# Optimization experiments

Measured on AMD Instinct MI355X. Metric: run time of the kernel, lower is better.

The kernel has to match this reference:

```python
import jax, jax.numpy as jnp
import numpy as np

STEPS = 4
EMB = 128
HEADS = 3
NUM_GRAPHS = 64
NODES_PER = 64
N = NUM_GRAPHS * NODES_PER
E_SPARSE = N * 16
DATA_LENS = [NODES_PER] * NUM_GRAPHS


def _complete_edge_index(data_lens):
    # dense_to_sparse(complete_matrix) -> all (i,j) pairs within each block,
    # including self loops (diagonal of complete_matrix is 1).
    srcs, dsts = [], []
    start = 0
    for l in data_lens:
        idx = np.arange(start, start + l)
        srcs.append(np.repeat(idx, l))
        dsts.append(np.tile(idx, l))
        start += l
    return np.stack([np.concatenate(srcs), np.concatenate(dsts)]).astype(np.int32)


def leaky(x, slope=0.01):
    return jnp.where(x >= 0, x, slope * x)


def setup_inputs() -> dict:
    key = jax.random.key(0)
    ks = jax.random.split(key, 16)
    s = 0.05
    edge_complete = jnp.asarray(_complete_edge_index(DATA_LENS))
    # sparse edge_index: random edges within each graph
    src_local = jax.random.randint(ks[1], (E_SPARSE,), 0, NODES_PER)
    dst_local = jax.random.randint(ks[2], (E_SPARSE,), 0, NODES_PER)
    gid = jnp.repeat(jnp.arange(NUM_GRAPHS), E_SPARSE // NUM_GRAPHS) * NODES_PER
    edge_index = jnp.stack([src_local + gid, dst_local + gid]).astype(jnp.int32)
    batch_ind = jnp.repeat(jnp.arange(NUM_GRAPHS), NODES_PER).astype(jnp.int32)
    return {
        "x": jax.random.normal(ks[0], (N, EMB), jnp.float32),
        "edge_index": edge_index,
        "batch_ind": batch_ind,
        "edge_complete": edge_complete,
        "Wm": jax.random.normal(ks[3], (STEPS, EMB, EMB)) * s,
        "bm": jnp.zeros((STEPS, EMB)),
        "Wa": jax.random.normal(ks[4], (STEPS, 3 * EMB, EMB)) * s,
        "ba": jnp.zeros((STEPS, EMB)),
        "Wl": jax.random.normal(ks[5], (STEPS - 1, EMB, HEADS * EMB)) * s,
        "bl": jnp.zeros((STEPS - 1, HEADS * EMB)),
        "Wr": jax.random.normal(ks[6], (STEPS - 1, EMB, HEADS * EMB)) * s,
        "br": jnp.zeros((STEPS - 1, HEADS * EMB)),
        "att_w": jax.random.normal(ks[7], (STEPS - 1, HEADS, EMB)) * s,
        "att_bias": jnp.zeros((STEPS - 1, EMB)),
    }


def _graphnet(x, x_att, batch_ind, src, dst, Wm, bm, Wa, ba):
    # message: f_mess(x_j)  (edge_attr is None in this model)
    m = leaky(x[src] @ Wm + bm)                               # [E, D]
    agg = jax.ops.segment_max(m, dst, num_segments=x.shape[0])
    agg = jnp.where(jnp.isneginf(agg), 0.0, agg)              # PyG fills empty with 0
    xg = x_att[batch_ind]                                     # [N, D]
    z = jnp.concatenate([x, xg, agg], axis=1)                 # [N, 3D]
    return leaky(z @ Wa + ba) + x


def _gatv2(x, src, dst, Wl, bl, Wr, br, att, bias):
    n = x.shape[0]
    xl = (x @ Wl + bl).reshape(n, HEADS, EMB)                 # source transform
    xr = (x @ Wr + br).reshape(n, HEADS, EMB)                 # target transform
    e = leaky(xl[src] + xr[dst], 0.2)                         # [E, H, D]
    logits = jnp.einsum('ehd,hd->eh', e, att)                 # [E, H]
    mx = jax.ops.segment_max(logits, dst, num_segments=n)
    mx = jnp.where(jnp.isneginf(mx), 0.0, mx)
    alpha = jnp.exp(logits - mx[dst])
    denom = jax.ops.segment_sum(alpha, dst, num_segments=n)
    alpha = alpha / denom[dst]                                # softmax over incoming edges
    out = jax.ops.segment_sum(alpha[:, :, None] * xl[src], dst, num_segments=n)
    return out.mean(axis=1) + bias                            # concat=False -> head mean


def reference(x, edge_index, batch_ind, edge_complete, Wm, bm, Wa, ba, Wl, bl, Wr, br, att_w, att_bias):
    src, dst = edge_index[0], edge_index[1]
    csrc, cdst = edge_complete[0], edge_complete[1]
    x_att = jnp.zeros((NUM_GRAPHS, EMB), x.dtype)
    for i in range(STEPS):
        x = _graphnet(x, x_att, batch_ind, src, dst, Wm[i], bm[i], Wa[i], ba[i])
        if i < STEPS - 1:
            x_att_nodes = leaky(_gatv2(x, csrc, cdst, Wl[i], bl[i], Wr[i], br[i], att_w[i], att_bias[i]))
            # original indexes xg = x_att[batch_ind]; x_att here is per-node, so
            # emulate torch semantics: x_att has len(x) rows, indexed by batch_ind.
            x_att = x_att_nodes
        # note: in original, x_att has shape [len(x), emb]; xg = x_att[batch_ind]
    return x


if __name__ == "__main__":
    out = reference(**setup_inputs())
    print(out.shape)
```

## Files before the change

### kernel.cpp

```cpp
#include <hip/hip_runtime.h>
#include <math.h>

#define D 128
#define GB 64
#define BT 1024
#define ZP 264
#define XLP 74

typedef __attribute__((ext_vector_type(8))) short bf16x8;
typedef __attribute__((ext_vector_type(4))) float f32x4;
typedef __attribute__((ext_vector_type(4))) unsigned u32x4;

__device__ __forceinline__ float leaky01(float v) { return v >= 0.f ? v : 0.01f * v; }
__device__ __forceinline__ unsigned short f2bf(float f) {
    unsigned u = __float_as_uint(f);
    u += 0x7FFFu + ((u >> 16) & 1u);
    return (unsigned short)(u >> 16);
}
__device__ __forceinline__ float bf2f(unsigned short s) {
    return __uint_as_float(((unsigned)s) << 16);
}

__device__ __forceinline__ void st_sys_u32(unsigned* p, unsigned v) {
    asm volatile("global_store_dword %0, %1, off sc0 sc1" :: "v"(p), "v"(v) : "memory");
}
__device__ __forceinline__ void st_sys_u128(unsigned* p, u32x4 v) {
    asm volatile("global_store_dwordx4 %0, %1, off sc0 sc1" :: "v"(p), "v"(v) : "memory");
}
__device__ __forceinline__ unsigned ld_sys_u32(const unsigned* p) {
    unsigned v;
    asm volatile("global_load_dword %0, %1, off sc0 sc1\n\ts_waitcnt vmcnt(0)"
                 : "=v"(v) : "v"(p) : "memory");
    return v;
}
__device__ __forceinline__ u32x4 ld_sys_u128(const unsigned* p) {
    u32x4 v;
    asm volatile("global_load_dwordx4 %0, %1, off sc0 sc1\n\ts_waitcnt vmcnt(0)"
                 : "=v"(v) : "v"(p) : "memory");
    return v;
}
__device__ __forceinline__ void waitst() { asm volatile("s_waitcnt vmcnt(0)" ::: "memory"); }

__global__ void k_wconv(const float* __restrict__ Wm, const float* __restrict__ Wa,
                        const float* __restrict__ Wl, const float* __restrict__ Wr,
                        unsigned short* __restrict__ Wmt, unsigned short* __restrict__ Wat,
                        unsigned short* __restrict__ Wlt, unsigned short* __restrict__ Wrt,
                        unsigned* __restrict__ flags) {
    int gid = blockIdx.x * blockDim.x + threadIdx.x;
    if (blockIdx.x == 0 && threadIdx.x < 8) st_sys_u32(&flags[threadIdx.x], 0u);
    if (gid < 16384) {
        int o = gid * 4;
        int s = o >> 14, rem = o & 16383, n = rem >> 7, k0 = rem & 127;
        const float* src = Wm + (size_t)s * 16384;
        unsigned short* dst = Wmt + o;
#pragma unroll
        for (int j = 0; j < 4; ++j) dst[j] = f2bf(src[(size_t)(k0 + j) * 128 + n]);
    } else if (gid < 49152) {
        int o = (gid - 16384) * 4;
        int s = o >> 15, rem = o & 32767, n = rem >> 8, k0 = rem & 255;
        int row = (k0 < 128) ? k0 : (k0 + 128);
        const float* src = Wa + (size_t)s * 49152;
        unsigned short* dst = Wat + o;
#pragma unroll
        for (int j = 0; j < 4; ++j) dst[j] = f2bf(src[(size_t)(row + j) * 128 + n]);
    } else if (gid < 86016) {
        int o = (gid - 49152) * 4;
        int s = o / 49152, rem = o % 49152, n = rem >> 7, k0 = rem & 127;
        const float* src = Wl + (size_t)s * 49152;
        unsigned short* dst = Wlt + o;
#pragma unroll
        for (int j = 0; j < 4; ++j) dst[j] = f2bf(src[(size_t)(k0 + j) * 384 + n]);
    } else if (gid < 122880) {
        int o = (gid - 86016) * 4;
        unsigned short* dst = Wrt + o;
#pragma unroll
        for (int j = 0; j < 4; ++j) dst[j] = f2bf(Wr[(size_t)o + j]);
    }
}

struct Args {
    const float* x0;
    const int* e_src; const int* e_dst;
    const unsigned short *Wmt, *Wat, *Wlt, *Wrt;
    const float *Wa, *bm, *ba, *bl, *br, *att_w, *att_bias;
    unsigned short* xg0;
    unsigned* flagX;
    float* out;
};

__global__ __launch_bounds__(BT) void k_mega(Args p) {
    const int tid = threadIdx.x, bid = blockIdx.x, g = bid;
    const int wave = tid >> 6, lane = tid & 63;
    const int m16 = lane & 15, kg = lane >> 4;
    const int wtile = wave >> 1;
    const int half = wave & 1;
    const int col = wtile * 16 + m16;

    __shared__ unsigned short zsb[64][ZP];
    __shared__ unsigned short hs[64][128];
    __shared__ unsigned short xl3[3][128][XLP];
    __shared__ float red[4608];
    __shared__ unsigned mlo[64], mhi[64];
    __shared__ float att_s[3][D];
    __shared__ float br_s[384];
    __shared__ float xgrow[D];

    unsigned short (*xg_s)[128] = (unsigned short(*)[128])&hs[0][0];

    if (tid < 64) { mlo[tid] = 0u; mhi[tid] = 0u; }
    __syncthreads();
    {
        int i0 = g * 1024 + tid;
        int s1 = p.e_src[i0] - g * 64, d1 = p.e_dst[i0] - g * 64;
        atomicOr(s1 < 32 ? &mlo[d1] : &mhi[d1], 1u << (s1 & 31));
    }

    float xreg[8];
    {
        const float* xp = p.x0 + (size_t)g * 64 * D;
#pragma unroll
        for (int i = 0; i < 2; ++i) {
            int mt = half * 2 + i;
#pragma unroll
            for (int r = 0; r < 4; ++r)
                xreg[i * 4 + r] = xp[(mt * 16 + kg * 4 + r) * D + col];
        }
    }
    __syncthreads();

    for (int step = 0; step < 4; ++step) {
        if (step > 0 && tid < 128) {
            float accO = red[3840 + tid] + red[3840 + 128 + tid] + red[3840 + 256 + tid]
                       + red[3840 + 384 + tid] + red[3840 + 512 + tid] + red[3840 + 640 + tid];
            xgrow[tid] = leaky01(accO * (1.f / 3.f) + p.att_bias[(step - 1) * 128 + tid]);
        }
#pragma unroll
        for (int i = 0; i < 2; ++i) {
            int mt = half * 2 + i;
#pragma unroll
            for (int r = 0; r < 4; ++r) zsb[mt * 16 + kg * 4 + r][col] = f2bf(xreg[i * 4 + r]);
        }
        if (step < 3 && tid < 384) {
            att_s[tid >> 7][tid & 127] = p.att_w[step * 384 + tid];
            br_s[tid] = p.br[step * 384 + tid];
        }
        __syncthreads();

        {
            const unsigned short* Wb = p.Wmt + ((size_t)(step * 128 + col) * 128 + kg * 8);
            bf16x8 bB[4];
#pragma unroll
            for (int kt = 0; kt < 4; ++kt) bB[kt] = *(const bf16x8*)(Wb + kt * 32);
            float bb = p.bm[step * 128 + col];
#pragma unroll
            for (int i = 0; i < 2; ++i) {
                int mt = half * 2 + i;
                f32x4 acc = {0.f, 0.f, 0.f, 0.f};
#pragma unroll
                for (int kt = 0; kt < 4; ++kt) {
                    bf16x8 a = *(const bf16x8*)&zsb[mt * 16 + m16][kt * 32 + kg * 8];
                    acc = __builtin_amdgcn_mfma_f32_16x16x32_bf16(a, bB[kt], acc, 0, 0, 0);
                }
#pragma unroll
                for (int r = 0; r < 4; ++r)
                    hs[mt * 16 + kg * 4 + r][col] = f2bf(leaky01(acc[r] + bb));
            }
        }
        __syncthreads();

        bf16x8 wat[8];
        {
            const unsigned short* WbU = p.Wat + ((size_t)(step * 128 + col) * 256 + kg * 8);
#pragma unroll
            for (int kt = 0; kt < 8; ++kt) wat[kt] = *(const bf16x8*)(WbU + kt * 32);
        }
        if (step > 0) {
            int n = tid & 127, q = tid >> 7;
            float a = 0.f;
            const float* Wmid = p.Wa + (size_t)step * 49152 + (size_t)(128 + q * 16) * 128 + n;
#pragma unroll 8
            for (int k2 = 0; k2 < 16; ++k2) a += xgrow[q * 16 + k2] * Wmid[(size_t)k2 * 128];
            red[q * 128 + n] = a;
        }
        {
            int r0 = wave * 4;
#pragma unroll
            for (int r = 0; r < 4; ++r) {
                int row = r0 + r;
                unsigned lo = (unsigned)__builtin_amdgcn_readfirstlane((int)mlo[row]);
                unsigned hi = (unsigned)__builtin_amdgcn_readfirstlane((int)mhi[row]);
                unsigned long long mk = (((unsigned long long)hi) << 32) | lo;
                float m0 = -INFINITY, m1 = -INFINITY;
                unsigned long long t = mk;
                while (t) {
                    int s = __builtin_ctzll(t);
                    t &= t - 1;
                    unsigned hv = *(const unsigned*)&hs[s][lane * 2];
                    m0 = fmaxf(m0, bf2f((unsigned short)(hv & 0xffffu)));
                    m1 = fmaxf(m1, bf2f((unsigned short)(hv >> 16)));
                }
                unsigned pk = mk ? (((unsigned)f2bf(m1) << 16) | (unsigned)f2bf(m0)) : 0u;
                *(unsigned*)&zsb[row][128 + lane * 2] = pk;
            }
        }
        __syncthreads();

        {
            float yg = 0.f;
            if (step > 0) {
#pragma unroll
                for (int q2 = 0; q2 < 8; ++q2) yg += red[q2 * 128 + col];
            }
            float extra = p.ba[step * 128 + col] + yg;
#pragma unroll
            for (int i = 0; i < 2; ++i) {
                int mt = half * 2 + i;
                f32x4 acc = {0.f, 0.f, 0.f, 0.f};
#pragma unroll
                for (int kt = 0; kt < 8; ++kt) {
                    bf16x8 a = *(const bf16x8*)&zsb[mt * 16 + m16][kt * 32 + kg * 8];
                    acc = __builtin_amdgcn_mfma_f32_16x16x32_bf16(a, wat[kt], acc, 0, 0, 0);
                }
#pragma unroll
                for (int r = 0; r < 4; ++r) {
                    float v = leaky01(acc[r] + extra) + xreg[i * 4 + r];
                    xreg[i * 4 + r] = v;
                    if (step == 3) p.out[((size_t)g * 64 + mt * 16 + kg * 4 + r) * D + col] = v;
                }
            }
            if (bid == 0 && step < 3) {
#pragma unroll
                for (int i = 0; i < 2; ++i) {
                    int mt = half * 2 + i;
#pragma unroll
                    for (int r = 0; r < 4; ++r) {
                        int row = mt * 16 + kg * 4 + r;
                        unsigned off = (unsigned)(row * 256 + col * 2) ^ (unsigned)((row & 7) << 4);
                        *(unsigned short*)((char*)&xg_s[0][0] + off) = f2bf(xreg[i * 4 + r]);
                    }
                }
            }
        }
        __syncthreads();

        if (step < 3) {
            unsigned short* xg0g = p.xg0 + (size_t)step * 8192;
            if (bid == 0) {
                {
                    unsigned boff = (unsigned)tid * 16;
                    int row = tid >> 4;
                    u32x4 v = *(u32x4*)((char*)&xg_s[0][0] + (boff ^ (unsigned)((row & 7) << 4)));
                    st_sys_u128((unsigned*)((char*)xg0g + boff), v);
                }
                waitst();
                __syncthreads();
                if (tid == 0) st_sys_u32(p.flagX + step, 1u);
                __syncthreads();
            } else {
                if (tid == 0) {
                    int it = 0;
                    while (ld_sys_u32(p.flagX + step) == 0 && it++ < (1 << 22))
                        __builtin_amdgcn_s_sleep(2);
                }
                __syncthreads();
                {
                    unsigned boff = (unsigned)tid * 16;
                    int row = tid >> 4;
                    u32x4 v = ld_sys_u128((const unsigned*)((const char*)xg0g + boff));
                    *(u32x4*)((char*)&xg_s[0][0] + (boff ^ (unsigned)((row & 7) << 4))) = v;
                }
                __syncthreads();
            }

            for (int h = 0; h < 3; ++h) {
                const unsigned short* Wb = p.Wlt + ((size_t)(step * 384 + h * 128 + col) * 128 + kg * 8);
                bf16x8 bB[4];
#pragma unroll
                for (int kt = 0; kt < 4; ++kt) bB[kt] = *(const bf16x8*)(Wb + kt * 32);
                float bb = p.bl[step * 384 + h * 128 + col];
#pragma unroll
                for (int i = 0; i < 2; ++i) {
                    int mt = half * 2 + i;
                    f32x4 acc = {0.f, 0.f, 0.f, 0.f};
#pragma unroll
                    for (int kt = 0; kt < 4; ++kt) {
                        int row = mt * 16 + m16;
                        unsigned off = (unsigned)(row * 256 + (kt * 32 + kg * 8) * 2) ^ (unsigned)((row & 7) << 4);
                        bf16x8 a = *(const bf16x8*)((const char*)&xg_s[0][0] + off);
                        acc = __builtin_amdgcn_mfma_f32_16x16x32_bf16(a, bB[kt], acc, 0, 0, 0);
                    }
                    int s0 = mt * 16 + kg * 4;
                    unsigned pk0 = (unsigned)f2bf(acc[0] + bb) | ((unsigned)f2bf(acc[1] + bb) << 16);
                    unsigned pk1 = (unsigned)f2bf(acc[2] + bb) | ((unsigned)f2bf(acc[3] + bb) << 16);
                    *(unsigned*)&xl3[h][col][s0] = pk0;
                    *(unsigned*)&xl3[h][col][s0 + 2] = pk1;
                }
            }
            if (tid < 768) {
                int q = (tid >= 384) ? 1 : 0;
                int n3 = tid - q * 384;
                int h = n3 >> 7, n = n3 & 127;
                float a = 0.f;
                const unsigned short* Wrp = p.Wrt + (size_t)step * 49152 + (size_t)(q * 64) * 384 + h * 128 + n;
#pragma unroll 8
                for (int k2 = 0; k2 < 64; ++k2) {
                    int k = q * 64 + k2;
                    unsigned b = ((unsigned)(g * 256 + k * 2)) ^ (unsigned)((g & 7) << 4);
                    float xv = bf2f(*(const unsigned short*)((const char*)&xg_s[0][0] + b));
                    a += xv * bf2f(Wrp[(size_t)k2 * 384]);
                }
                red[3072 + q * 384 + n3] = a;
            }
            __syncthreads();

            {
                int kb = wave * 8;
#pragma unroll
                for (int h = 0; h < 3; ++h) {
                    float part = 0.f;
#pragma unroll
                    for (int kk = 0; kk < 8; ++kk) {
                        int k = kb + kk;
                        float xr = red[3072 + h * 128 + k] + red[3072 + 384 + h * 128 + k]
                                 + br_s[h * 128 + k];
                        float t = bf2f(xl3[h][k][lane]) + xr;
                        t = (t >= 0.f) ? t : 0.2f * t;
                        part += att_s[h][k] * t;
                    }
                    red[(h * 16 + wave) * 64 + lane] = part;
                }
            }
            __syncthreads();

            {
                int q = tid >> 7, c = tid & 127;
                if (q < 6) {
                    int h = q >> 1, sq = q & 1;
                    float lg = 0.f;
#pragma unroll
                    for (int w2 = 0; w2 < 16; ++w2) lg += red[(h * 16 + w2) * 64 + lane];
                    float mx = lg;
#pragma unroll
                    for (int o = 32; o > 0; o >>= 1) mx = fmaxf(mx, __shfl_xor(mx, o));
                    float a = __expf(lg - mx), sm = a;
#pragma unroll
                    for (int o = 32; o > 0; o >>= 1) sm += __shfl_xor(sm, o);
                    float alpha = a / sm;
                    float pv = 0.f;
#pragma unroll
                    for (int s2 = 0; s2 < 32; ++s2) {
                        int s = sq * 32 + s2;
                        float as = __shfl(alpha, s);
                        pv += as * bf2f(xl3[h][c][s]);
                    }
                    red[3840 + q * 128 + c] = pv;
                }
            }
            __syncthreads();
        }
    }
}

extern "C" void kernel_launch(void* const* d_in, const int* in_sizes, int n_in,
                              void* d_out, int out_size, void* d_ws, size_t ws_size,
                              hipStream_t stream) {
    (void)n_in; (void)out_size; (void)ws_size;
    const float* x_in     = (const float*)d_in[0];
    const int*   edge_idx = (const int*)d_in[1];
    const float* Wm  = (const float*)d_in[4];
    const float* bm  = (const float*)d_in[5];
    const float* Wa  = (const float*)d_in[6];
    const float* ba  = (const float*)d_in[7];
    const float* Wl  = (const float*)d_in[8];
    const float* bl  = (const float*)d_in[9];
    const float* Wr  = (const float*)d_in[10];
    const float* br  = (const float*)d_in[11];
    const float* att_w    = (const float*)d_in[12];
    const float* att_bias = (const float*)d_in[13];
    const int E = in_sizes[1] / 2;

    char* ws = (char*)d_ws;
    size_t off = 0;
    auto alloc = [&](size_t bytes) { void* pp = ws + off; off += (bytes + 255) & ~size_t(255); return pp; };
    unsigned short* xg0 = (unsigned short*)alloc((size_t)3 * 64 * 128 * 2);
    unsigned short* Wmt = (unsigned short*)alloc((size_t)4 * 128 * 128 * 2);
    unsigned short* Wat = (unsigned short*)alloc((size_t)4 * 128 * 256 * 2);
    unsigned short* Wlt = (unsigned short*)alloc((size_t)3 * 384 * 128 * 2);
    unsigned short* Wrt = (unsigned short*)alloc((size_t)3 * 128 * 384 * 2);
    unsigned* flags     = (unsigned*)alloc(8 * 4);

    k_wconv<<<480, 256, 0, stream>>>(Wm, Wa, Wl, Wr, Wmt, Wat, Wlt, Wrt, flags);

    Args a;
    a.x0 = x_in;
    a.e_src = edge_idx;
    a.e_dst = edge_idx + E;
    a.Wmt = Wmt; a.Wat = Wat; a.Wlt = Wlt; a.Wrt = Wrt;
    a.Wa = Wa; a.bm = bm; a.ba = ba; a.bl = bl; a.br = br;
    a.att_w = att_w; a.att_bias = att_bias;
    a.xg0 = xg0; a.flagX = flags;
    a.out = (float*)d_out;
    void* kargs[] = { (void*)&a };
    (void)hipLaunchCooperativeKernel((void*)k_mega, dim3(GB), dim3(BT), kargs, 0, stream);
}
```

Before: 128.5 us.

## Overlap GATv2 attention of previous step with next step's message GEMM via wave specialization

```diff
diff --git a/kernel.cpp b/kernel.cpp
--- a/kernel.cpp
+++ b/kernel.cpp
@@ -92,20 +92,24 @@
     const int tid = threadIdx.x, bid = blockIdx.x, g = bid;
     const int wave = tid >> 6, lane = tid & 63;
     const int m16 = lane & 15, kg = lane >> 4;
-    const int wtile = wave >> 1;
-    const int half = wave & 1;
+    const int wtile = wave >> 1, half = wave & 1;
     const int col = wtile * 16 + m16;
+    const bool gA = wave < 8;
+    const int wA = wave;
+    const int wB = wave - 8;
+    const int tid2 = tid - 512;
 
     __shared__ unsigned short zsb[64][ZP];
     __shared__ unsigned short hs[64][128];
     __shared__ unsigned short xl3[3][128][XLP];
     __shared__ float red[4608];
+    __shared__ unsigned short xgs[8192];
     __shared__ unsigned mlo[64], mhi[64];
     __shared__ float att_s[3][D];
     __shared__ float br_s[384];
     __shared__ float xgrow[D];
 
-    unsigned short (*xg_s)[128] = (unsigned short(*)[128])&hs[0][0];
+    char* const xgsB = (char*)&xgs[0];
 
     if (tid < 64) { mlo[tid] = 0u; mhi[tid] = 0u; }
     __syncthreads();
@@ -126,35 +130,26 @@
                 xreg[i * 4 + r] = xp[(mt * 16 + kg * 4 + r) * D + col];
         }
     }
+#pragma unroll
+    for (int i = 0; i < 2; ++i) {
+        int mt = half * 2 + i;
+#pragma unroll
+        for (int r = 0; r < 4; ++r) zsb[mt * 16 + kg * 4 + r][col] = f2bf(xreg[i * 4 + r]);
+    }
     __syncthreads();
 
     for (int step = 0; step < 4; ++step) {
-        if (step > 0 && tid < 128) {
-            float accO = red[3840 + tid] + red[3840 + 128 + tid] + red[3840 + 256 + tid]
-                       + red[3840 + 384 + tid] + red[3840 + 512 + tid] + red[3840 + 640 + tid];
-            xgrow[tid] = leaky01(accO * (1.f / 3.f) + p.att_bias[(step - 1) * 128 + tid]);
-        }
-#pragma unroll
-        for (int i = 0; i < 2; ++i) {
-            int mt = half * 2 + i;
-#pragma unroll
-            for (int r = 0; r < 4; ++r) zsb[mt * 16 + kg * 4 + r][col] = f2bf(xreg[i * 4 + r]);
-        }
-        if (step < 3 && tid < 384) {
-            att_s[tid >> 7][tid & 127] = p.att_w[step * 384 + tid];
-            br_s[tid] = p.br[step * 384 + tid];
-        }
-        __syncthreads();
-
-        {
-            const unsigned short* Wb = p.Wmt + ((size_t)(step * 128 + col) * 128 + kg * 8);
+        const int sg = step - 1;
+
+        if (gA) {
+            const int colA = wA * 16 + m16;
+            const unsigned short* Wb = p.Wmt + ((size_t)(step * 128 + colA) * 128 + kg * 8);
             bf16x8 bB[4];
 #pragma unroll
             for (int kt = 0; kt < 4; ++kt) bB[kt] = *(const bf16x8*)(Wb + kt * 32);
-            float bb = p.bm[step * 128 + col];
-#pragma unroll
-            for (int i = 0; i < 2; ++i) {
-                int mt = half * 2 + i;
+            float bb = p.bm[step * 128 + colA];
+#pragma unroll
+            for (int mt = 0; mt < 4; ++mt) {
                 f32x4 acc = {0.f, 0.f, 0.f, 0.f};
 #pragma unroll
                 for (int kt = 0; kt < 4; ++kt) {
@@ -163,29 +158,66 @@
                 }
 #pragma unroll
                 for (int r = 0; r < 4; ++r)
-                    hs[mt * 16 + kg * 4 + r][col] = f2bf(leaky01(acc[r] + bb));
-            }
-        }
-        __syncthreads();
-
-        bf16x8 wat[8];
-        {
-            const unsigned short* WbU = p.Wat + ((size_t)(step * 128 + col) * 256 + kg * 8);
-#pragma unroll
-            for (int kt = 0; kt < 8; ++kt) wat[kt] = *(const bf16x8*)(WbU + kt * 32);
-        }
-        if (step > 0) {
-            int n = tid & 127, q = tid >> 7;
-            float a = 0.f;
-            const float* Wmid = p.Wa + (size_t)step * 49152 + (size_t)(128 + q * 16) * 128 + n;
+                    hs[mt * 16 + kg * 4 + r][colA] = f2bf(leaky01(acc[r] + bb));
+            }
+        } else if (step > 0) {
+            const int colB = wB * 16 + m16;
+            for (int h = 0; h < 3; ++h) {
+                const unsigned short* Wb = p.Wlt + ((size_t)(sg * 384 + h * 128 + colB) * 128 + kg * 8);
+                bf16x8 bB[4];
+#pragma unroll
+                for (int kt = 0; kt < 4; ++kt) bB[kt] = *(const bf16x8*)(Wb + kt * 32);
+                float bb = p.bl[sg * 384 + h * 128 + colB];
+#pragma unroll
+                for (int mt = 0; mt < 4; ++mt) {
+                    f32x4 acc = {0.f, 0.f, 0.f, 0.f};
+#pragma unroll
+                    for (int kt = 0; kt < 4; ++kt) {
+                        int row = mt * 16 + m16;
+                        unsigned off = (unsigned)(row * 256 + (kt * 32 + kg * 8) * 2) ^ (unsigned)((row & 7) << 4);
+                        bf16x8 a = *(const bf16x8*)(xgsB + off);
+                        acc = __builtin_amdgcn_mfma_f32_16x16x32_bf16(a, bB[kt], acc, 0, 0, 0);
+                    }
+                    int s0 = mt * 16 + kg * 4;
+                    unsigned pk0 = (unsigned)f2bf(acc[0] + bb) | ((unsigned)f2bf(acc[1] + bb) << 16);
+                    unsigned pk1 = (unsigned)f2bf(acc[2] + bb) | ((unsigned)f2bf(acc[3] + bb) << 16);
+                    *(unsigned*)&xl3[h][colB][s0] = pk0;
+                    *(unsigned*)&xl3[h][colB][s0 + 2] = pk1;
+                }
+            }
+            {
+                int slot = tid2;
+                int q = slot >= 384; int n3 = slot - q * 384; int h = n3 >> 7, n = n3 & 127;
+                float a = 0.f;
+                const unsigned short* Wrp = p.Wrt + (size_t)sg * 49152 + (size_t)(q * 64) * 384 + h * 128 + n;
 #pragma unroll 8
-            for (int k2 = 0; k2 < 16; ++k2) a += xgrow[q * 16 + k2] * Wmid[(size_t)k2 * 128];
-            red[q * 128 + n] = a;
-        }
-        {
-            int r0 = wave * 4;
-#pragma unroll
-            for (int r = 0; r < 4; ++r) {
+                for (int k2 = 0; k2 < 64; ++k2) {
+                    int k = q * 64 + k2;
+                    unsigned b = ((unsigned)(g * 256 + k * 2)) ^ (unsigned)((g & 7) << 4);
+                    a += bf2f(*(const unsigned short*)(xgsB + b)) * bf2f(Wrp[(size_t)k2 * 384]);
+                }
+                red[3072 + slot] = a;
+            }
+            if (tid2 < 256) {
+                int slot = 512 + tid2;
+                int n3 = slot - 384; int h = n3 >> 7, n = n3 & 127;
+                float a = 0.f;
+                const unsigned short* Wrp = p.Wrt + (size_t)sg * 49152 + (size_t)64 * 384 + h * 128 + n;
+#pragma unroll 8
+                for (int k2 = 0; k2 < 64; ++k2) {
+                    int k = 64 + k2;
+                    unsigned b = ((unsigned)(g * 256 + k * 2)) ^ (unsigned)((g & 7) << 4);
+                    a += bf2f(*(const unsigned short*)(xgsB + b)) * bf2f(Wrp[(size_t)k2 * 384]);
+                }
+                red[3072 + slot] = a;
+            }
+        }
+        __syncthreads();
+
+        if (gA) {
+            int r0 = wA * 8;
+#pragma unroll
+            for (int r = 0; r < 8; ++r) {
                 int row = r0 + r;
                 unsigned lo = (unsigned)__builtin_amdgcn_readfirstlane((int)mlo[row]);
                 unsigned hi = (unsigned)__builtin_amdgcn_readfirstlane((int)mhi[row]);
@@ -202,6 +234,92 @@
                 unsigned pk = mk ? (((unsigned)f2bf(m1) << 16) | (unsigned)f2bf(m0)) : 0u;
                 *(unsigned*)&zsb[row][128 + lane * 2] = pk;
             }
+        } else if (step > 0) {
+#pragma unroll
+            for (int h = 0; h < 3; ++h)
+#pragma unroll
+                for (int j = 0; j < 2; ++j) {
+                    float part = 0.f;
+#pragma unroll
+                    for (int kk = 0; kk < 8; ++kk) {
+                        int k = wB * 16 + j * 8 + kk;
+                        float xr = red[3072 + h * 128 + k] + red[3072 + 384 + h * 128 + k]
+                                 + br_s[h * 128 + k];
+                        float t = bf2f(xl3[h][k][lane]) + xr;
+                        t = (t >= 0.f) ? t : 0.2f * t;
+                        part += att_s[h][k] * t;
+                    }
+                    red[(h * 16 + wB * 2 + j) * 64 + lane] = part;
+                }
+        }
+        __syncthreads();
+
+        if (!gA && step > 0) {
+            {
+                int q = tid2 >> 7, c = tid2 & 127, ln = tid2 & 63;
+                int h = q >> 1, sq = q & 1;
+                float lg = 0.f;
+#pragma unroll
+                for (int w2 = 0; w2 < 16; ++w2) lg += red[(h * 16 + w2) * 64 + ln];
+                float mx = lg;
+#pragma unroll
+                for (int o = 32; o > 0; o >>= 1) mx = fmaxf(mx, __shfl_xor(mx, o));
+                float a = __expf(lg - mx), sm = a;
+#pragma unroll
+                for (int o = 32; o > 0; o >>= 1) sm += __shfl_xor(sm, o);
+                float alpha = a / sm;
+                float pv = 0.f;
+#pragma unroll
+                for (int s2 = 0; s2 < 32; ++s2) {
+                    int s = sq * 32 + s2;
+                    pv += __shfl(alpha, s) * bf2f(xl3[h][c][s]);
+                }
+                red[3840 + q * 128 + c] = pv;
+            }
+            if (tid2 < 256) {
+                int q = 4 + (tid2 >> 7), c = tid2 & 127, ln = tid2 & 63;
+                int h = q >> 1, sq = q & 1;
+                float lg = 0.f;
+#pragma unroll
+                for (int w2 = 0; w2 < 16; ++w2) lg += red[(h * 16 + w2) * 64 + ln];
+                float mx = lg;
+#pragma unroll
+                for (int o = 32; o > 0; o >>= 1) mx = fmaxf(mx, __shfl_xor(mx, o));
+                float a = __expf(lg - mx), sm = a;
+#pragma unroll
+                for (int o = 32; o > 0; o >>= 1) sm += __shfl_xor(sm, o);
+                float alpha = a / sm;
+                float pv = 0.f;
+#pragma unroll
+                for (int s2 = 0; s2 < 32; ++s2) {
+                    int s = sq * 32 + s2;
+                    pv += __shfl(alpha, s) * bf2f(xl3[h][c][s]);
+                }
+                red[3840 + q * 128 + c] = pv;
+            }
+        }
+        __syncthreads();
+
+        if (step > 0 && tid < 128) {
+            float accO = red[3840 + tid] + red[3840 + 128 + tid] + red[3840 + 256 + tid]
+                       + red[3840 + 384 + tid] + red[3840 + 512 + tid] + red[3840 + 640 + tid];
+            xgrow[tid] = leaky01(accO * (1.f / 3.f) + p.att_bias[sg * 128 + tid]);
+        }
+        __syncthreads();
+
+        bf16x8 wat[8];
+        {
+            const unsigned short* WbU = p.Wat + ((size_t)(step * 128 + col) * 256 + kg * 8);
+#pragma unroll
+            for (int kt = 0; kt < 8; ++kt) wat[kt] = *(const bf16x8*)(WbU + kt * 32);
+        }
+        if (step > 0) {
+            int n = tid & 127, q = tid >> 7;
+            float a = 0.f;
+            const float* Wmid = p.Wa + (size_t)step * 49152 + (size_t)(128 + q * 16) * 128 + n;
+#pragma unroll 8
+            for (int k2 = 0; k2 < 16; ++k2) a += xgrow[q * 16 + k2] * Wmid[(size_t)k2 * 128];
+            red[q * 128 + n] = a;
         }
         __syncthreads();
 
@@ -236,7 +354,7 @@
                     for (int r = 0; r < 4; ++r) {
                         int row = mt * 16 + kg * 4 + r;
                         unsigned off = (unsigned)(row * 256 + col * 2) ^ (unsigned)((row & 7) << 4);
-                        *(unsigned short*)((char*)&xg_s[0][0] + off) = f2bf(xreg[i * 4 + r]);
+                        *(unsigned short*)(xgsB + off) = f2bf(xreg[i * 4 + r]);
                     }
                 }
             }
@@ -249,13 +367,12 @@
                 {
                     unsigned boff = (unsigned)tid * 16;
                     int row = tid >> 4;
-                    u32x4 v = *(u32x4*)((char*)&xg_s[0][0] + (boff ^ (unsigned)((row & 7) << 4)));
+                    u32x4 v = *(u32x4*)(xgsB + (boff ^ (unsigned)((row & 7) << 4)));
                     st_sys_u128((unsigned*)((char*)xg0g + boff), v);
                 }
                 waitst();
                 __syncthreads();
                 if (tid == 0) st_sys_u32(p.flagX + step, 1u);
-                __syncthreads();
             } else {
                 if (tid == 0) {
                     int it = 0;
@@ -267,94 +384,18 @@
                     unsigned boff = (unsigned)tid * 16;
                     int row = tid >> 4;
                     u32x4 v = ld_sys_u128((const unsigned*)((const char*)xg0g + boff));
-                    *(u32x4*)((char*)&xg_s[0][0] + (boff ^ (unsigned)((row & 7) << 4))) = v;
-                }
-                __syncthreads();
-            }
-
-            for (int h = 0; h < 3; ++h) {
-                const unsigned short* Wb = p.Wlt + ((size_t)(step * 384 + h * 128 + col) * 128 + kg * 8);
-                bf16x8 bB[4];
-#pragma unroll
-                for (int kt = 0; kt < 4; ++kt) bB[kt] = *(const bf16x8*)(Wb + kt * 32);
-                float bb = p.bl[step * 384 + h * 128 + col];
-#pragma unroll
-                for (int i = 0; i < 2; ++i) {
-                    int mt = half * 2 + i;
-                    f32x4 acc = {0.f, 0.f, 0.f, 0.f};
-#pragma unroll
-                    for (int kt = 0; kt < 4; ++kt) {
-                        int row = mt * 16 + m16;
-                        unsigned off = (unsigned)(row * 256 + (kt * 32 + kg * 8) * 2) ^ (unsigned)((row & 7) << 4);
-                        bf16x8 a = *(const bf16x8*)((const char*)&xg_s[0][0] + off);
-                        acc = __builtin_amdgcn_mfma_f32_16x16x32_bf16(a, bB[kt], acc, 0, 0, 0);
-                    }
-                    int s0 = mt * 16 + kg * 4;
-                    unsigned pk0 = (unsigned)f2bf(acc[0] + bb) | ((unsigned)f2bf(acc[1] + bb) << 16);
-                    unsigned pk1 = (unsigned)f2bf(acc[2] + bb) | ((unsigned)f2bf(acc[3] + bb) << 16);
-                    *(unsigned*)&xl3[h][col][s0] = pk0;
-                    *(unsigned*)&xl3[h][col][s0 + 2] = pk1;
-                }
-            }
-            if (tid < 768) {
-                int q = (tid >= 384) ? 1 : 0;
-                int n3 = tid - q * 384;
-                int h = n3 >> 7, n = n3 & 127;
-                float a = 0.f;
-                const unsigned short* Wrp = p.Wrt + (size_t)step * 49152 + (size_t)(q * 64) * 384 + h * 128 + n;
-#pragma unroll 8
-                for (int k2 = 0; k2 < 64; ++k2) {
-                    int k = q * 64 + k2;
-                    unsigned b = ((unsigned)(g * 256 + k * 2)) ^ (unsigned)((g & 7) << 4);
-                    float xv = bf2f(*(const unsigned short*)((const char*)&xg_s[0][0] + b));
-                    a += xv * bf2f(Wrp[(size_t)k2 * 384]);
-                }
-                red[3072 + q * 384 + n3] = a;
-            }
-            __syncthreads();
-
-            {
-                int kb = wave * 8;
-#pragma unroll
-                for (int h = 0; h < 3; ++h) {
-                    float part = 0.f;
-#pragma unroll
-                    for (int kk = 0; kk < 8; ++kk) {
-                        int k = kb + kk;
-                        float xr = red[3072 + h * 128 + k] + red[3072 + 384 + h * 128 + k]
-                                 + br_s[h * 128 + k];
-                        float t = bf2f(xl3[h][k][lane]) + xr;
-                        t = (t >= 0.f) ? t : 0.2f * t;
-                        part += att_s[h][k] * t;
-                    }
-                    red[(h * 16 + wave) * 64 + lane] = part;
-                }
-            }
-            __syncthreads();
-
-            {
-                int q = tid >> 7, c = tid & 127;
-                if (q < 6) {
-                    int h = q >> 1, sq = q & 1;
-                    float lg = 0.f;
-#pragma unroll
-                    for (int w2 = 0; w2 < 16; ++w2) lg += red[(h * 16 + w2) * 64 + lane];
-                    float mx = lg;
-#pragma unroll
-                    for (int o = 32; o > 0; o >>= 1) mx = fmaxf(mx, __shfl_xor(mx, o));
-                    float a = __expf(lg - mx), sm = a;
-#pragma unroll
-                    for (int o = 32; o > 0; o >>= 1) sm += __shfl_xor(sm, o);
-                    float alpha = a / sm;
-                    float pv = 0.f;
-#pragma unroll
-                    for (int s2 = 0; s2 < 32; ++s2) {
-                        int s = sq * 32 + s2;
-                        float as = __shfl(alpha, s);
-                        pv += as * bf2f(xl3[h][c][s]);
-                    }
-                    red[3840 + q * 128 + c] = pv;
-                }
+                    *(u32x4*)(xgsB + (boff ^ (unsigned)((row & 7) << 4))) = v;
+                }
+            }
+#pragma unroll
+            for (int i = 0; i < 2; ++i) {
+                int mt = half * 2 + i;
+#pragma unroll
+                for (int r = 0; r < 4; ++r) zsb[mt * 16 + kg * 4 + r][col] = f2bf(xreg[i * 4 + r]);
+            }
+            if (tid < 384) {
+                att_s[tid >> 7][tid & 127] = p.att_w[step * 384 + tid];
+                br_s[tid] = p.br[step * 384 + tid];
             }
             __syncthreads();
         }
```

Result: slower. 136.2 us (+6.0%).
